# Optimization experiments

Hardware: AMD Instinct MI355X
Metric: run time of the kernel (lower is better)

## Reference

```python
import jax, jax.numpy as jnp
import numpy as np

B, T, D, K = 64, 4096, 90, 32
LOG2PI = 1.8378770664093453


def setup_inputs() -> dict:
    key = jax.random.key(0)
    k1, k2, k3, k4, k5 = jax.random.split(key, 5)
    X = jax.random.normal(k1, (B, T, D), dtype=jnp.float32)
    state_priors = jax.random.uniform(k2, (K,), dtype=jnp.float32)
    transition_matrix = jax.random.uniform(k3, (K, K), dtype=jnp.float32)
    mu = jax.random.normal(k4, (K, D), dtype=jnp.float32) * 0.5
    log_var = jax.random.normal(k5, (K, D), dtype=jnp.float32) * 0.1
    return {"X": X, "state_priors": state_priors,
            "transition_matrix": transition_matrix, "mu": mu, "log_var": log_var}


def _emission_logprobs(X, mu, log_var):
    # Diagonal-Gaussian log density per state: (B,T,K)
    # expand (x-mu)^2*inv_var to avoid materializing a (B,T,K,D) tensor
    inv_var = jnp.exp(-log_var)                                   # (K,D)
    quad = (jnp.einsum('btd,kd->btk', X * X, inv_var)
            - 2.0 * jnp.einsum('btd,kd->btk', X, mu * inv_var)
            + jnp.sum(mu * mu * inv_var, axis=-1))                # (B,T,K)
    return -0.5 * (quad + jnp.sum(log_var, axis=-1) + D * LOG2PI)


def reference(X, state_priors, transition_matrix, mu, log_var):
    log_A = jax.nn.log_softmax(transition_matrix, axis=1)   # (K,K)
    log_pi = jax.nn.log_softmax(state_priors, axis=0)       # (K,)
    em = _emission_logprobs(X, mu, log_var)                 # (B,T,K)

    log_alpha0 = log_pi + em[:, 0, :]                       # (B,K)

    def step(log_alpha, e_t):
        # log_alpha: (B,K), e_t: (B,K)
        la = e_t + jax.nn.logsumexp(log_alpha[:, :, None] + log_A[None], axis=1)
        return la, None

    em_rest = jnp.swapaxes(em[:, 1:, :], 0, 1)              # (T-1,B,K)
    log_alpha_T, _ = jax.lax.scan(step, log_alpha0, em_rest)
    # sum over subjects of logsumexp over states at final timestep
    return jnp.sum(jax.nn.logsumexp(log_alpha_T, axis=-1))
```

## Files before the change

kernel.cpp:

```cpp
#include <hip/hip_runtime.h>
#include <stdint.h>

#define B_ 64
#define T_ 4096
#define D_ 90
#define K_ 32
#define CH_ 32
#define F_  128

typedef float f32x16 __attribute__((ext_vector_type(16)));
typedef __bf16 bf16x8 __attribute__((ext_vector_type(8)));

#define WS_A     0
#define WS_PI    1024
#define WS_C0    1056
#define WS_WF    1088
#define WS_EACC  4160
#define WS_MS    12352
#define WS_E0    20544
#define WS_PE    21568
#define WS_PM    22080
#define WS_Q     284224

__device__ __forceinline__ int perm_r(int r) {
  int t2 = (r >> 2) & 3;
  return r + ((t2 == 1) ? 4 : (t2 == 2) ? -4 : 0);
}
__device__ __forceinline__ uint32_t pk2(float hi, float lo) {
  return __builtin_amdgcn_perm(__float_as_uint(hi), __float_as_uint(lo), 0x07060302u);
}
__device__ __forceinline__ uint32_t rnd_pk(float hi, float lo) {
  uint32_t uh = __float_as_uint(hi) + 0x8000u;
  uint32_t ul = __float_as_uint(lo) + 0x8000u;
  return __builtin_amdgcn_perm(uh, ul, 0x07060302u);
}
__device__ __forceinline__ float bf2f(ushort u) {
  return __uint_as_float(((uint32_t)u) << 16);
}
__device__ __forceinline__ bf16x8 mkbf(uint32_t a, uint32_t b, uint32_t c, uint32_t d) {
  union { uint32_t u[4]; bf16x8 v; } x;
  x.u[0] = a; x.u[1] = b; x.u[2] = c; x.u[3] = d;
  return x.v;
}

__global__ __launch_bounds__(1024) void prep_kernel(
    const float* __restrict__ priors, const float* __restrict__ trans,
    const float* __restrict__ mu, const float* __restrict__ lv,
    float* __restrict__ ws) {
  int tid = threadIdx.x;
  {
    float v = trans[tid];
    float m = v;
    #pragma unroll
    for (int mk = 16; mk; mk >>= 1) m = fmaxf(m, __shfl_xor(m, mk));
    float e = expf(v - m);
    float s = e;
    #pragma unroll
    for (int mk = 16; mk; mk >>= 1) s += __shfl_xor(s, mk);
    ws[WS_A + tid] = e / s;
  }
  if (tid < 32) {
    float v = priors[tid];
    float m = v;
    #pragma unroll
    for (int mk = 16; mk; mk >>= 1) m = fmaxf(m, __shfl_xor(m, mk));
    float e = expf(v - m);
    float s = e;
    #pragma unroll
    for (int mk = 16; mk; mk >>= 1) s += __shfl_xor(s, mk);
    ws[WS_PI + tid] = e / s;
  }
  for (int i = tid; i < 6144; i += 1024) {
    int j = i & 7, l = (i >> 3) & 63, cm = i >> 9;
    int c = cm >> 1, mat = cm & 1;
    int h = l >> 5, nn = l & 31;
    int d = 16 * c + 8 * h + j;
    float v = 0.0f;
    if (d < D_) {
      float ivd = expf(-lv[nn * D_ + d]);
      v = (mat == 0) ? -0.5f * ivd : mu[nn * D_ + d] * ivd;
    }
    ((ushort*)(ws + WS_WF))[i] = (ushort)((__float_as_uint(v) + 0x8000u) >> 16);
  }
  if (tid < 32) {
    float s = 0.0f;
    for (int d = 0; d < D_; ++d) {
      float l  = lv[tid * D_ + d];
      float iv = expf(-l);
      float m_ = mu[tid * D_ + d];
      s += m_ * m_ * iv + l;
    }
    ws[WS_C0 + tid] = -0.5f * (s + (float)D_ * 1.8378770664093453f);
  }
}

__global__ __launch_bounds__(256, 6) void fused_kernel(const float* __restrict__ X,
                                                       float* __restrict__ ws) {
  __shared__ ushort sh[4][32 * 104];
  int tid = threadIdx.x;
  int l = tid & 63, w = tid >> 6;
  int n = l & 31, h = l >> 5;
  int tB = blockIdx.x << 7;
  const float4* Xg = (const float4*)(X + (size_t)tB * D_);
  #pragma unroll
  for (int it = 0; it < 12; ++it) {
    int i = tid + (it << 8);
    if (i < 2880) {
      float4 v = Xg[i];
      int g = i / 720;
      int f = (i - g * 720) * 4;
      uint32_t d0 = rnd_pk(v.y, v.x);
      uint32_t d1 = rnd_pk(v.w, v.z);
      int r0 = f / 90;        int c0_ = f - r0 * 90;
      int r1 = (f + 2) / 90;  int c1_ = (f + 2) - r1 * 90;
      *(uint32_t*)&sh[g][r0 * 104 + c0_] = d0;
      *(uint32_t*)&sh[g][r1 * 104 + c1_] = d1;
    }
  }
  for (int i = tid; i < 896; i += 256) {
    int r = i / 7;
    int d = 90 + 2 * (i - r * 7);
    *(uint32_t*)&sh[r >> 5][(r & 31) * 104 + d] = 0u;
  }
  const uint4* wfp = (const uint4*)((const ushort*)(ws + WS_WF));
  uint4 wf[12];
  #pragma unroll
  for (int cm = 0; cm < 12; ++cm) wf[cm] = wfp[cm * 64 + l];
  float c0 = ws[WS_C0 + n];
  __syncthreads();

  int t0 = tB + (w << 5);
  int b  = t0 >> 12;
  int bc = t0 >> 5;
  const ushort* xrow = &sh[w][n * 104];
  f32x16 acc1, acc2;
  #pragma unroll
  for (int r = 0; r < 16; ++r) { acc1[r] = 0.0f; acc2[r] = 0.0f; }
  #pragma unroll
  for (int c = 0; c < 6; ++c) {
    union { uint4 u; bf16x8 v; } xb;
    xb.u = *(const uint4*)(xrow + 16 * c + 8 * h);
    float x[8];
    #pragma unroll
    for (int j = 0; j < 8; ++j) {
      uint32_t uu = ((const uint32_t*)&xb.u)[j >> 1];
      x[j] = bf2f((j & 1) ? (ushort)(uu >> 16) : (ushort)(uu & 0xFFFF));
    }
    union { uint32_t u[4]; bf16x8 v; } x2b;
    #pragma unroll
    for (int r = 0; r < 4; ++r)
      x2b.u[r] = rnd_pk(x[2*r+1] * x[2*r+1], x[2*r] * x[2*r]);
    union { uint4 u; bf16x8 v; } w2, w1;
    w2.u = wf[c * 2]; w1.u = wf[c * 2 + 1];
    acc1 = __builtin_amdgcn_mfma_f32_32x32x16_bf16(xb.v,  w1.v, acc1, 0, 0, 0);
    acc2 = __builtin_amdgcn_mfma_f32_32x32x16_bf16(x2b.v, w2.v, acc2, 0, 0, 0);
  }
  float em[16], mrow[16];
  #pragma unroll
  for (int r = 0; r < 16; ++r) {
    float v = acc1[r] + acc2[r] + c0;
    em[r] = v;
    float m = v;
    #pragma unroll
    for (int mk = 1; mk <= 16; mk <<= 1) m = fmaxf(m, __shfl_xor(m, mk));
    mrow[r] = m;
  }
  ushort* Ew = sh[w];
  #pragma unroll
  for (int q = 0; q < 4; ++q) {
    float e0 = exp2f((em[4*q]   - mrow[4*q])   * 1.44269504088896f);
    float e1 = exp2f((em[4*q+1] - mrow[4*q+1]) * 1.44269504088896f);
    float e2 = exp2f((em[4*q+2] - mrow[4*q+2]) * 1.44269504088896f);
    float e3 = exp2f((em[4*q+3] - mrow[4*q+3]) * 1.44269504088896f);
    uint2 d;
    d.x = rnd_pk(e1, e0);
    d.y = rnd_pk(e3, e2);
    *(uint2*)(Ew + n * 40 + 8 * q + 4 * h) = d;
    if (q == 0 && h == 0 && (t0 & (T_ - 1)) == 0)
      ((ushort*)(ws + WS_E0))[b * K_ + n] = (ushort)(d.x & 0xFFFF);
  }
  float msum = 0.0f;
  #pragma unroll
  for (int r = 0; r < 16; ++r) msum += mrow[r];
  msum += __shfl_xor(msum, 32);
  if (l == 0) ws[WS_MS + bc] = msum;

  int col = perm_r(n);
  const float* A = ws + WS_A;
  float astat[16];
  #pragma unroll
  for (int j = 0; j < 8; ++j) {
    astat[j]     = A[(8 * h + j) * K_ + col];
    astat[8 + j] = A[(16 + 8 * h + j) * K_ + col];
  }
  uint32_t q[8];
  #pragma unroll
  for (int r = 0; r < 4; ++r) {
    int s0 = 8 * h + 2 * r;
    uint32_t lo = (s0 == n)     ? 0x3F80u : 0u;
    uint32_t hi = (s0 + 1 == n) ? 0x3F80u : 0u;
    q[r] = lo | (hi << 16);
    int s2 = s0 + 16;
    lo = (s2 == n)     ? 0x3F80u : 0u;
    hi = (s2 + 1 == n) ? 0x3F80u : 0u;
    q[4 + r] = lo | (hi << 16);
  }
  int eacc = 0;
  const f32x16 z = {0.f,0.f,0.f,0.f,0.f,0.f,0.f,0.f,0.f,0.f,0.f,0.f,0.f,0.f,0.f,0.f};
  f32x16 acc;
  #pragma unroll
  for (int r = 0; r < 16; ++r) acc[r] = 0.0f;

  auto step = [&](float e0) {
    uint32_t au[8];
    #pragma unroll
    for (int r = 0; r < 4; ++r) {
      au[r]     = pk2(astat[2 * r + 1] * e0, astat[2 * r] * e0);
      au[4 + r] = pk2(astat[8 + 2 * r + 1] * e0, astat[8 + 2 * r] * e0);
    }
    bf16x8 alo = mkbf(au[0], au[1], au[2], au[3]);
    bf16x8 ahi = mkbf(au[4], au[5], au[6], au[7]);
    bf16x8 qlo = mkbf(q[0], q[1], q[2], q[3]);
    bf16x8 qhi = mkbf(q[4], q[5], q[6], q[7]);
    acc = __builtin_amdgcn_mfma_f32_32x32x16_bf16(alo, qlo, z, 0, 0, 0);
    acc = __builtin_amdgcn_mfma_f32_32x32x16_bf16(ahi, qhi, acc, 0, 0, 0);
    #pragma unroll
    for (int r = 0; r < 4; ++r) {
      q[r]     = pk2(acc[2 * r + 1], acc[2 * r]);
      q[4 + r] = pk2(acc[8 + 2 * r + 1], acc[8 + 2 * r]);
    }
  };
  auto renorm = [&]() {
    float m = acc[0];
    #pragma unroll
    for (int r = 1; r < 16; ++r) m = fmaxf(m, acc[r]);
    #pragma unroll
    for (int mk = 1; mk <= 32; mk <<= 1) m = fmaxf(m, __shfl_xor(m, mk));
    int ex;
    frexpf(m, &ex);
    float sc = ldexpf(1.0f, -ex);
    eacc += ex;
    #pragma unroll
    for (int r = 0; r < 16; ++r) acc[r] *= sc;
    #pragma unroll
    for (int r = 0; r < 4; ++r) {
      q[r]     = pk2(acc[2 * r + 1], acc[2 * r]);
      q[4 + r] = pk2(acc[8 + 2 * r + 1], acc[8 + 2 * r]);
    }
  };

  const ushort* Eb = sh[w] + col * 40;
  int g0 = 0;
  if ((t0 & (T_ - 1)) == 0) {
    uint4 ev = *(const uint4*)(Eb);
    #pragma unroll
    for (int j = 1; j < 8; ++j) {
      uint32_t u = ((const uint32_t*)&ev)[j >> 1];
      step(bf2f((j & 1) ? (ushort)(u >> 16) : (ushort)(u & 0xFFFF)));
    }
    renorm();
    g0 = 1;
  }
  for (int g = g0; g < CH_ / 8; ++g) {
    uint4 ev = *(const uint4*)(Eb + 8 * g);
    #pragma unroll
    for (int j = 0; j < 8; ++j) {
      uint32_t u = ((const uint32_t*)&ev)[j >> 1];
      step(bf2f((j & 1) ? (ushort)(u >> 16) : (ushort)(u & 0xFFFF)));
    }
    renorm();
  }
  ushort* Qo = (ushort*)(ws + WS_Q) + (size_t)bc * (K_ * K_);
  #pragma unroll
  for (int r = 0; r < 16; ++r) {
    int m_ = (r & 3) + 8 * (r >> 2) + 4 * h;
    Qo[perm_r(m_) * K_ + n] = (ushort)(__float_as_uint(acc[r]) >> 16);
  }
  if (l == 0) ((int*)ws)[WS_EACC + bc] = eacc;
}

__global__ __launch_bounds__(64) void combine1_kernel(float* __restrict__ ws) {
  int l = threadIdx.x;
  int h = l >> 5, n = l & 31;
  int bw = blockIdx.x;
  int b = bw >> 3, w = bw & 7;
  int row = perm_r(n);
  const ushort* Qb = (const ushort*)(ws + WS_Q) + (size_t)(b * F_ + w * 16) * (K_ * K_);
  int eacc;
  {
    const int* ea = ((const int*)ws) + WS_EACC + b * F_ + w * 16;
    int v = (l < 16) ? ea[l] : 0;
    #pragma unroll
    for (int mk = 1; mk <= 8; mk <<= 1) v += __shfl_xor(v, mk);
    eacc = __shfl(v, 0);
  }
  uint32_t q[8];
  #pragma unroll
  for (int r = 0; r < 4; ++r) {
    int s0 = 8 * h + 2 * r;
    uint32_t lo = (s0 == n)     ? 0x3F80u : 0u;
    uint32_t hi = (s0 + 1 == n) ? 0x3F80u : 0u;
    q[r] = lo | (hi << 16);
    int s2 = s0 + 16;
    lo = (s2 == n)     ? 0x3F80u : 0u;
    hi = (s2 + 1 == n) ? 0x3F80u : 0u;
    q[4 + r] = lo | (hi << 16);
  }
  f32x16 acc;
  #pragma unroll
  for (int r = 0; r < 16; ++r) acc[r] = 0.0f;
  const f32x16 z = {0.f,0.f,0.f,0.f,0.f,0.f,0.f,0.f,0.f,0.f,0.f,0.f,0.f,0.f,0.f,0.f};

  auto lmul = [&](uint4 lo, uint4 hi) {
    bf16x8 alo = mkbf(lo.x, lo.y, lo.z, lo.w);
    bf16x8 ahi = mkbf(hi.x, hi.y, hi.z, hi.w);
    bf16x8 qlo = mkbf(q[0], q[1], q[2], q[3]);
    bf16x8 qhi = mkbf(q[4], q[5], q[6], q[7]);
    acc = __builtin_amdgcn_mfma_f32_32x32x16_bf16(alo, qlo, z, 0, 0, 0);
    acc = __builtin_amdgcn_mfma_f32_32x32x16_bf16(ahi, qhi, acc, 0, 0, 0);
    #pragma unroll
    for (int r = 0; r < 4; ++r) {
      q[r]     = pk2(acc[2 * r + 1], acc[2 * r]);
      q[4 + r] = pk2(acc[8 + 2 * r + 1], acc[8 + 2 * r]);
    }
  };
  auto renorm = [&]() {
    float m = acc[0];
    #pragma unroll
    for (int r = 1; r < 16; ++r) m = fmaxf(m, acc[r]);
    #pragma unroll
    for (int mk = 1; mk <= 32; mk <<= 1) m = fmaxf(m, __shfl_xor(m, mk));
    int ex;
    frexpf(m, &ex);
    float sc = ldexpf(1.0f, -ex);
    eacc += ex;
    #pragma unroll
    for (int r = 0; r < 16; ++r) acc[r] *= sc;
    #pragma unroll
    for (int r = 0; r < 4; ++r) {
      q[r]     = pk2(acc[2 * r + 1], acc[2 * r]);
      q[4 + r] = pk2(acc[8 + 2 * r + 1], acc[8 + 2 * r]);
    }
  };

  uint4 rlo[4], rhi[4];
  #pragma unroll
  for (int p = 0; p < 4; ++p) {
    const ushort* Mc = Qb + (size_t)p * (K_ * K_) + row * K_;
    rlo[p] = *(const uint4*)(Mc + 8 * h);
    rhi[p] = *(const uint4*)(Mc + 16 + 8 * h);
  }
  #pragma unroll
  for (int c = 0; c < 16; ++c) {
    lmul(rlo[c & 3], rhi[c & 3]);
    if (c + 4 < 16) {
      const ushort* Mc = Qb + (size_t)(c + 4) * (K_ * K_) + row * K_;
      rlo[c & 3] = *(const uint4*)(Mc + 8 * h);
      rhi[c & 3] = *(const uint4*)(Mc + 16 + 8 * h);
    }
    if ((c & 3) == 3) renorm();
  }
  ushort* pmq = (ushort*)(ws + WS_PM) + (size_t)bw * (K_ * K_);
  #pragma unroll
  for (int r = 0; r < 16; ++r) {
    int m_ = (r & 3) + 8 * (r >> 2) + 4 * h;
    pmq[perm_r(m_) * K_ + n] = (ushort)(__float_as_uint(acc[r]) >> 16);
  }
  if (l == 0) ((int*)ws)[WS_PE + bw] = eacc;
}

__global__ __launch_bounds__(64) void combine2_kernel(float* __restrict__ ws,
                                                      float* __restrict__ out) {
  int l = threadIdx.x;
  int h = l >> 5, n = l & 31;
  int b = blockIdx.x;
  int row = perm_r(n);
  float alpha0 = ws[WS_PI + n] * bf2f(((const ushort*)(ws + WS_E0))[b * K_ + n]);
  float msm = ws[WS_MS + b * 128 + l] + ws[WS_MS + b * 128 + 64 + l];
  uint32_t q[8];
  #pragma unroll
  for (int r = 0; r < 4; ++r) {
    int s0 = 8 * h + 2 * r;
    uint32_t lo = (s0 == n)     ? 0x3F80u : 0u;
    uint32_t hi = (s0 + 1 == n) ? 0x3F80u : 0u;
    q[r] = lo | (hi << 16);
    int s2 = s0 + 16;
    lo = (s2 == n)     ? 0x3F80u : 0u;
    hi = (s2 + 1 == n) ? 0x3F80u : 0u;
    q[4 + r] = lo | (hi << 16);
  }
  f32x16 acc;
  #pragma unroll
  for (int r = 0; r < 16; ++r) acc[r] = 0.0f;
  const f32x16 z = {0.f,0.f,0.f,0.f,0.f,0.f,0.f,0.f,0.f,0.f,0.f,0.f,0.f,0.f,0.f,0.f};
  const ushort* pmq = (const ushort*)(ws + WS_PM) + (size_t)b * 8 * (K_ * K_);
  #pragma unroll
  for (int p = 0; p < 8; ++p) {
    const ushort* base = pmq + p * (K_ * K_) + row * K_;
    uint4 lo = *(const uint4*)(base + 8 * h);
    uint4 hi = *(const uint4*)(base + 16 + 8 * h);
    bf16x8 alo = mkbf(lo.x, lo.y, lo.z, lo.w);
    bf16x8 ahi = mkbf(hi.x, hi.y, hi.z, hi.w);
    bf16x8 qlo = mkbf(q[0], q[1], q[2], q[3]);
    bf16x8 qhi = mkbf(q[4], q[5], q[6], q[7]);
    acc = __builtin_amdgcn_mfma_f32_32x32x16_bf16(alo, qlo, z, 0, 0, 0);
    acc = __builtin_amdgcn_mfma_f32_32x32x16_bf16(ahi, qhi, acc, 0, 0, 0);
    #pragma unroll
    for (int r = 0; r < 4; ++r) {
      q[r]     = pk2(acc[2 * r + 1], acc[2 * r]);
      q[4 + r] = pk2(acc[8 + 2 * r + 1], acc[8 + 2 * r]);
    }
  }
  int et = (l < 8) ? ((const int*)ws)[WS_PE + b * 8 + l] : 0;
  #pragma unroll
  for (int mk = 1; mk <= 4; mk <<= 1) et += __shfl_xor(et, mk);
  et = __shfl(et, 0);
  float part = 0.0f;
  #pragma unroll
  for (int r = 0; r < 16; ++r) part += acc[r];
  part *= alpha0;
  #pragma unroll
  for (int mk = 1; mk <= 32; mk <<= 1) part += __shfl_xor(part, mk);
  #pragma unroll
  for (int mk = 32; mk; mk >>= 1) msm += __shfl_xor(msm, mk);
  if (l == 0) {
    float res = logf(part) + (float)et * 0.69314718055994531f + msm;
    atomicAdd(out, res);
  }
}

extern "C" void kernel_launch(void* const* d_in, const int* in_sizes, int n_in,
                              void* d_out, int out_size, void* d_ws, size_t ws_size,
                              hipStream_t stream) {
  (void)in_sizes; (void)n_in; (void)out_size; (void)ws_size;
  const float* X      = (const float*)d_in[0];
  const float* priors = (const float*)d_in[1];
  const float* trans  = (const float*)d_in[2];
  const float* mu     = (const float*)d_in[3];
  const float* lv     = (const float*)d_in[4];
  float* ws  = (float*)d_ws;
  float* out = (float*)d_out;
  hipMemsetAsync(out, 0, sizeof(float), stream);
  prep_kernel<<<1, 1024, 0, stream>>>(priors, trans, mu, lv, ws);
  fused_kernel<<<B_ * T_ / 128, 256, 0, stream>>>(X, ws);
  combine1_kernel<<<B_ * 8, 64, 0, stream>>>(ws);
  combine2_kernel<<<B_, 64, 0, stream>>>(ws, out);
}
```

Before: 185.7 us.

## Fold first combine level into fused kernel and merge combine stages

The fused kernel now multiplies the four per-warp 32x32 chunk transfer matrices inside each block through shared memory. It writes one matrix per block, cutting global workspace traffic and removing the combine1 launch. A single 256-thread combine kernel per batch reduces 32 block matrices in two levels. X is loaded directly from global memory into MFMA operands instead of staging through shared memory, the memset is folded into the kernel, and occupancy is raised to 8 blocks per SIMD. The changes add a block-wide sync plus serial tail work on warp 0, and bring uncoalesced strided X loads.

```diff
diff --git a/kernel.cpp b/kernel.cpp
--- a/kernel.cpp
+++ b/kernel.cpp
@@ -7,6 +7,7 @@
 #define K_ 32
 #define CH_ 32
 #define F_  128
+#define NB_ 2048
 
 typedef float f32x16 __attribute__((ext_vector_type(16)));
 typedef __bf16 bf16x8 __attribute__((ext_vector_type(8)));
@@ -18,9 +19,7 @@
 #define WS_EACC  4160
 #define WS_MS    12352
 #define WS_E0    20544
-#define WS_PE    21568
-#define WS_PM    22080
-#define WS_Q     284224
+#define WS_Q2    22080
 
 __device__ __forceinline__ int perm_r(int r) {
   int t2 = (r >> 2) & 3;
@@ -94,64 +93,41 @@
   }
 }
 
-__global__ __launch_bounds__(256, 6) void fused_kernel(const float* __restrict__ X,
-                                                       float* __restrict__ ws) {
-  __shared__ ushort sh[4][32 * 104];
+__global__ __launch_bounds__(256, 8) void fused_kernel(const float* __restrict__ X,
+                                                       float* __restrict__ ws,
+                                                       float* __restrict__ out) {
+  __shared__ __align__(16) ushort sh[4][1280];
+  __shared__ float msb[4];
+  __shared__ int   peb[4];
   int tid = threadIdx.x;
   int l = tid & 63, w = tid >> 6;
   int n = l & 31, h = l >> 5;
   int tB = blockIdx.x << 7;
-  const float4* Xg = (const float4*)(X + (size_t)tB * D_);
-  #pragma unroll
-  for (int it = 0; it < 12; ++it) {
-    int i = tid + (it << 8);
-    if (i < 2880) {
-      float4 v = Xg[i];
-      int g = i / 720;
-      int f = (i - g * 720) * 4;
-      uint32_t d0 = rnd_pk(v.y, v.x);
-      uint32_t d1 = rnd_pk(v.w, v.z);
-      int r0 = f / 90;        int c0_ = f - r0 * 90;
-      int r1 = (f + 2) / 90;  int c1_ = (f + 2) - r1 * 90;
-      *(uint32_t*)&sh[g][r0 * 104 + c0_] = d0;
-      *(uint32_t*)&sh[g][r1 * 104 + c1_] = d1;
-    }
-  }
-  for (int i = tid; i < 896; i += 256) {
-    int r = i / 7;
-    int d = 90 + 2 * (i - r * 7);
-    *(uint32_t*)&sh[r >> 5][(r & 31) * 104 + d] = 0u;
-  }
-  const uint4* wfp = (const uint4*)((const ushort*)(ws + WS_WF));
-  uint4 wf[12];
-  #pragma unroll
-  for (int cm = 0; cm < 12; ++cm) wf[cm] = wfp[cm * 64 + l];
-  float c0 = ws[WS_C0 + n];
-  __syncthreads();
-
   int t0 = tB + (w << 5);
   int b  = t0 >> 12;
-  int bc = t0 >> 5;
-  const ushort* xrow = &sh[w][n * 104];
+  if (blockIdx.x == 0 && tid == 0) *out = 0.0f;
+
+  const float* xr = X + (size_t)(t0 + n) * D_;
+  const uint4* wfp = (const uint4*)((const ushort*)(ws + WS_WF));
+  float c0 = ws[WS_C0 + n];
   f32x16 acc1, acc2;
   #pragma unroll
   for (int r = 0; r < 16; ++r) { acc1[r] = 0.0f; acc2[r] = 0.0f; }
   #pragma unroll
   for (int c = 0; c < 6; ++c) {
-    union { uint4 u; bf16x8 v; } xb;
-    xb.u = *(const uint4*)(xrow + 16 * c + 8 * h);
-    float x[8];
-    #pragma unroll
-    for (int j = 0; j < 8; ++j) {
-      uint32_t uu = ((const uint32_t*)&xb.u)[j >> 1];
-      x[j] = bf2f((j & 1) ? (ushort)(uu >> 16) : (ushort)(uu & 0xFFFF));
-    }
-    union { uint32_t u[4]; bf16x8 v; } x2b;
-    #pragma unroll
-    for (int r = 0; r < 4; ++r)
-      x2b.u[r] = rnd_pk(x[2*r+1] * x[2*r+1], x[2*r] * x[2*r]);
-    union { uint4 u; bf16x8 v; } w2, w1;
-    w2.u = wf[c * 2]; w1.u = wf[c * 2 + 1];
+    int s = 16 * c + 8 * h;
+    union { uint32_t u[4]; bf16x8 v; } xb, x2b;
+    #pragma unroll
+    for (int p = 0; p < 4; ++p) {
+      float2 v2;
+      if (s + 2 * p < D_) v2 = *(const float2*)(xr + s + 2 * p);
+      else { v2.x = 0.0f; v2.y = 0.0f; }
+      xb.u[p]  = rnd_pk(v2.y, v2.x);
+      x2b.u[p] = rnd_pk(v2.y * v2.y, v2.x * v2.x);
+    }
+    union { uint4 u; bf16x8 v; } w1, w2;
+    w2.u = wfp[(2 * c) * 64 + l];
+    w1.u = wfp[(2 * c + 1) * 64 + l];
     acc1 = __builtin_amdgcn_mfma_f32_32x32x16_bf16(xb.v,  w1.v, acc1, 0, 0, 0);
     acc2 = __builtin_amdgcn_mfma_f32_32x32x16_bf16(x2b.v, w2.v, acc2, 0, 0, 0);
   }
@@ -183,7 +159,7 @@
   #pragma unroll
   for (int r = 0; r < 16; ++r) msum += mrow[r];
   msum += __shfl_xor(msum, 32);
-  if (l == 0) ws[WS_MS + bc] = msum;
+  if (l == 0) msb[w] = msum;
 
   int col = perm_r(n);
   const float* A = ws + WS_A;
@@ -230,6 +206,19 @@
       q[4 + r] = pk2(acc[8 + 2 * r + 1], acc[8 + 2 * r]);
     }
   };
+  auto lmul = [&](uint4 lo, uint4 hi) {
+    bf16x8 alo = mkbf(lo.x, lo.y, lo.z, lo.w);
+    bf16x8 ahi = mkbf(hi.x, hi.y, hi.z, hi.w);
+    bf16x8 qlo = mkbf(q[0], q[1], q[2], q[3]);
+    bf16x8 qhi = mkbf(q[4], q[5], q[6], q[7]);
+    acc = __builtin_amdgcn_mfma_f32_32x32x16_bf16(alo, qlo, z, 0, 0, 0);
+    acc = __builtin_amdgcn_mfma_f32_32x32x16_bf16(ahi, qhi, acc, 0, 0, 0);
+    #pragma unroll
+    for (int r = 0; r < 4; ++r) {
+      q[r]     = pk2(acc[2 * r + 1], acc[2 * r]);
+      q[4 + r] = pk2(acc[8 + 2 * r + 1], acc[8 + 2 * r]);
+    }
+  };
   auto renorm = [&]() {
     float m = acc[0];
     #pragma unroll
@@ -270,31 +259,16 @@
     }
     renorm();
   }
-  ushort* Qo = (ushort*)(ws + WS_Q) + (size_t)bc * (K_ * K_);
+  ushort* Qw = sh[w];
   #pragma unroll
   for (int r = 0; r < 16; ++r) {
     int m_ = (r & 3) + 8 * (r >> 2) + 4 * h;
-    Qo[perm_r(m_) * K_ + n] = (ushort)(__float_as_uint(acc[r]) >> 16);
-  }
-  if (l == 0) ((int*)ws)[WS_EACC + bc] = eacc;
-}
-
-__global__ __launch_bounds__(64) void combine1_kernel(float* __restrict__ ws) {
-  int l = threadIdx.x;
-  int h = l >> 5, n = l & 31;
-  int bw = blockIdx.x;
-  int b = bw >> 3, w = bw & 7;
-  int row = perm_r(n);
-  const ushort* Qb = (const ushort*)(ws + WS_Q) + (size_t)(b * F_ + w * 16) * (K_ * K_);
-  int eacc;
-  {
-    const int* ea = ((const int*)ws) + WS_EACC + b * F_ + w * 16;
-    int v = (l < 16) ? ea[l] : 0;
-    #pragma unroll
-    for (int mk = 1; mk <= 8; mk <<= 1) v += __shfl_xor(v, mk);
-    eacc = __shfl(v, 0);
-  }
-  uint32_t q[8];
+    Qw[perm_r(m_) * 40 + n] = (ushort)(__float_as_uint(acc[r]) >> 16);
+  }
+  if (l == 0) peb[w] = eacc;
+  __syncthreads();
+  if (w != 0) return;
+
   #pragma unroll
   for (int r = 0; r < 4; ++r) {
     int s0 = 8 * h + 2 * r;
@@ -306,77 +280,45 @@
     hi = (s2 + 1 == n) ? 0x3F80u : 0u;
     q[4 + r] = lo | (hi << 16);
   }
-  f32x16 acc;
-  #pragma unroll
-  for (int r = 0; r < 16; ++r) acc[r] = 0.0f;
-  const f32x16 z = {0.f,0.f,0.f,0.f,0.f,0.f,0.f,0.f,0.f,0.f,0.f,0.f,0.f,0.f,0.f,0.f};
-
-  auto lmul = [&](uint4 lo, uint4 hi) {
-    bf16x8 alo = mkbf(lo.x, lo.y, lo.z, lo.w);
-    bf16x8 ahi = mkbf(hi.x, hi.y, hi.z, hi.w);
-    bf16x8 qlo = mkbf(q[0], q[1], q[2], q[3]);
-    bf16x8 qhi = mkbf(q[4], q[5], q[6], q[7]);
-    acc = __builtin_amdgcn_mfma_f32_32x32x16_bf16(alo, qlo, z, 0, 0, 0);
-    acc = __builtin_amdgcn_mfma_f32_32x32x16_bf16(ahi, qhi, acc, 0, 0, 0);
-    #pragma unroll
-    for (int r = 0; r < 4; ++r) {
-      q[r]     = pk2(acc[2 * r + 1], acc[2 * r]);
-      q[4 + r] = pk2(acc[8 + 2 * r + 1], acc[8 + 2 * r]);
-    }
-  };
-  auto renorm = [&]() {
-    float m = acc[0];
-    #pragma unroll
-    for (int r = 1; r < 16; ++r) m = fmaxf(m, acc[r]);
-    #pragma unroll
-    for (int mk = 1; mk <= 32; mk <<= 1) m = fmaxf(m, __shfl_xor(m, mk));
-    int ex;
-    frexpf(m, &ex);
-    float sc = ldexpf(1.0f, -ex);
-    eacc += ex;
-    #pragma unroll
-    for (int r = 0; r < 16; ++r) acc[r] *= sc;
-    #pragma unroll
-    for (int r = 0; r < 4; ++r) {
-      q[r]     = pk2(acc[2 * r + 1], acc[2 * r]);
-      q[4 + r] = pk2(acc[8 + 2 * r + 1], acc[8 + 2 * r]);
-    }
-  };
-
-  uint4 rlo[4], rhi[4];
+  eacc = peb[0] + peb[1] + peb[2] + peb[3];
+  float msm = msb[0] + msb[1] + msb[2] + msb[3];
   #pragma unroll
   for (int p = 0; p < 4; ++p) {
-    const ushort* Mc = Qb + (size_t)p * (K_ * K_) + row * K_;
-    rlo[p] = *(const uint4*)(Mc + 8 * h);
-    rhi[p] = *(const uint4*)(Mc + 16 + 8 * h);
-  }
-  #pragma unroll
-  for (int c = 0; c < 16; ++c) {
-    lmul(rlo[c & 3], rhi[c & 3]);
-    if (c + 4 < 16) {
-      const ushort* Mc = Qb + (size_t)(c + 4) * (K_ * K_) + row * K_;
-      rlo[c & 3] = *(const uint4*)(Mc + 8 * h);
-      rhi[c & 3] = *(const uint4*)(Mc + 16 + 8 * h);
-    }
-    if ((c & 3) == 3) renorm();
-  }
-  ushort* pmq = (ushort*)(ws + WS_PM) + (size_t)bw * (K_ * K_);
+    const ushort* base = sh[p] + col * 40;
+    uint4 lo = *(const uint4*)(base + 8 * h);
+    uint4 hi = *(const uint4*)(base + 16 + 8 * h);
+    lmul(lo, hi);
+  }
+  renorm();
+  ushort* Qo = (ushort*)(ws + WS_Q2) + (size_t)blockIdx.x * (K_ * K_);
   #pragma unroll
   for (int r = 0; r < 16; ++r) {
     int m_ = (r & 3) + 8 * (r >> 2) + 4 * h;
-    pmq[perm_r(m_) * K_ + n] = (ushort)(__float_as_uint(acc[r]) >> 16);
-  }
-  if (l == 0) ((int*)ws)[WS_PE + bw] = eacc;
-}
-
-__global__ __launch_bounds__(64) void combine2_kernel(float* __restrict__ ws,
+    Qo[perm_r(m_) * K_ + n] = (ushort)(__float_as_uint(acc[r]) >> 16);
+  }
+  if (l == 0) {
+    ((int*)ws)[WS_EACC + blockIdx.x] = eacc;
+    ws[WS_MS + blockIdx.x] = msm;
+  }
+}
+
+__global__ __launch_bounds__(256) void combine_kernel(float* __restrict__ ws,
                                                       float* __restrict__ out) {
-  int l = threadIdx.x;
+  __shared__ __align__(16) ushort pm[4][1280];
+  __shared__ int pe[4];
+  int tid = threadIdx.x;
+  int l = tid & 63, w = tid >> 6;
   int h = l >> 5, n = l & 31;
   int b = blockIdx.x;
   int row = perm_r(n);
-  float alpha0 = ws[WS_PI + n] * bf2f(((const ushort*)(ws + WS_E0))[b * K_ + n]);
-  float msm = ws[WS_MS + b * 128 + l] + ws[WS_MS + b * 128 + 64 + l];
+  int eacc;
+  {
+    const int* ea = ((const int*)ws) + WS_EACC + b * 32 + w * 8;
+    int v = (l < 8) ? ea[l] : 0;
+    #pragma unroll
+    for (int mk = 1; mk <= 4; mk <<= 1) v += __shfl_xor(v, mk);
+    eacc = __shfl(v, 0);
+  }
   uint32_t q[8];
   #pragma unroll
   for (int r = 0; r < 4; ++r) {
@@ -393,12 +335,8 @@
   #pragma unroll
   for (int r = 0; r < 16; ++r) acc[r] = 0.0f;
   const f32x16 z = {0.f,0.f,0.f,0.f,0.f,0.f,0.f,0.f,0.f,0.f,0.f,0.f,0.f,0.f,0.f,0.f};
-  const ushort* pmq = (const ushort*)(ws + WS_PM) + (size_t)b * 8 * (K_ * K_);
-  #pragma unroll
-  for (int p = 0; p < 8; ++p) {
-    const ushort* base = pmq + p * (K_ * K_) + row * K_;
-    uint4 lo = *(const uint4*)(base + 8 * h);
-    uint4 hi = *(const uint4*)(base + 16 + 8 * h);
+
+  auto lmul = [&](uint4 lo, uint4 hi) {
     bf16x8 alo = mkbf(lo.x, lo.y, lo.z, lo.w);
     bf16x8 ahi = mkbf(hi.x, hi.y, hi.z, hi.w);
     bf16x8 qlo = mkbf(q[0], q[1], q[2], q[3]);
@@ -410,19 +348,79 @@
       q[r]     = pk2(acc[2 * r + 1], acc[2 * r]);
       q[4 + r] = pk2(acc[8 + 2 * r + 1], acc[8 + 2 * r]);
     }
-  }
-  int et = (l < 8) ? ((const int*)ws)[WS_PE + b * 8 + l] : 0;
-  #pragma unroll
-  for (int mk = 1; mk <= 4; mk <<= 1) et += __shfl_xor(et, mk);
-  et = __shfl(et, 0);
+  };
+  auto renorm = [&]() {
+    float m = acc[0];
+    #pragma unroll
+    for (int r = 1; r < 16; ++r) m = fmaxf(m, acc[r]);
+    #pragma unroll
+    for (int mk = 1; mk <= 32; mk <<= 1) m = fmaxf(m, __shfl_xor(m, mk));
+    int ex;
+    frexpf(m, &ex);
+    float sc = ldexpf(1.0f, -ex);
+    eacc += ex;
+    #pragma unroll
+    for (int r = 0; r < 16; ++r) acc[r] *= sc;
+    #pragma unroll
+    for (int r = 0; r < 4; ++r) {
+      q[r]     = pk2(acc[2 * r + 1], acc[2 * r]);
+      q[4 + r] = pk2(acc[8 + 2 * r + 1], acc[8 + 2 * r]);
+    }
+  };
+
+  const ushort* Qb = (const ushort*)(ws + WS_Q2) + (size_t)(b * 32 + w * 8) * (K_ * K_);
+  #pragma unroll
+  for (int p = 0; p < 8; ++p) {
+    const ushort* Mc = Qb + (size_t)p * (K_ * K_) + row * K_;
+    uint4 lo = *(const uint4*)(Mc + 8 * h);
+    uint4 hi = *(const uint4*)(Mc + 16 + 8 * h);
+    lmul(lo, hi);
+    if ((p & 3) == 3) renorm();
+  }
+  #pragma unroll
+  for (int r = 0; r < 16; ++r) {
+    int m_ = (r & 3) + 8 * (r >> 2) + 4 * h;
+    pm[w][perm_r(m_) * 40 + n] = (ushort)(__float_as_uint(acc[r]) >> 16);
+  }
+  if (l == 0) pe[w] = eacc;
+  __syncthreads();
+  if (w != 0) return;
+
+  float alpha0 = ws[WS_PI + n] * bf2f(((const ushort*)(ws + WS_E0))[b * K_ + n]);
+  float msm;
+  {
+    float v = (l < 32) ? ws[WS_MS + b * 32 + l] : 0.0f;
+    #pragma unroll
+    for (int mk = 1; mk <= 32; mk <<= 1) v += __shfl_xor(v, mk);
+    msm = v;
+  }
+  #pragma unroll
+  for (int r = 0; r < 4; ++r) {
+    int s0 = 8 * h + 2 * r;
+    uint32_t lo = (s0 == n)     ? 0x3F80u : 0u;
+    uint32_t hi = (s0 + 1 == n) ? 0x3F80u : 0u;
+    q[r] = lo | (hi << 16);
+    int s2 = s0 + 16;
+    lo = (s2 == n)     ? 0x3F80u : 0u;
+    hi = (s2 + 1 == n) ? 0x3F80u : 0u;
+    q[4 + r] = lo | (hi << 16);
+  }
+  #pragma unroll
+  for (int r = 0; r < 16; ++r) acc[r] = 0.0f;
+  int et = pe[0] + pe[1] + pe[2] + pe[3];
+  #pragma unroll
+  for (int p = 0; p < 4; ++p) {
+    const ushort* base = pm[p] + row * 40;
+    uint4 lo = *(const uint4*)(base + 8 * h);
+    uint4 hi = *(const uint4*)(base + 16 + 8 * h);
+    lmul(lo, hi);
+  }
   float part = 0.0f;
   #pragma unroll
   for (int r = 0; r < 16; ++r) part += acc[r];
   part *= alpha0;
   #pragma unroll
   for (int mk = 1; mk <= 32; mk <<= 1) part += __shfl_xor(part, mk);
-  #pragma unroll
-  for (int mk = 32; mk; mk >>= 1) msm += __shfl_xor(msm, mk);
   if (l == 0) {
     float res = logf(part) + (float)et * 0.69314718055994531f + msm;
     atomicAdd(out, res);
@@ -440,9 +438,7 @@
   const float* lv     = (const float*)d_in[4];
   float* ws  = (float*)d_ws;
   float* out = (float*)d_out;
-  hipMemsetAsync(out, 0, sizeof(float), stream);
   prep_kernel<<<1, 1024, 0, stream>>>(priors, trans, mu, lv, ws);
-  fused_kernel<<<B_ * T_ / 128, 256, 0, stream>>>(X, ws);
-  combine1_kernel<<<B_ * 8, 64, 0, stream>>>(ws);
-  combine2_kernel<<<B_, 64, 0, stream>>>(ws, out);
-}
+  fused_kernel<<<NB_, 256, 0, stream>>>(X, ws, out);
+  combine_kernel<<<B_, 256, 0, stream>>>(ws, out);
+}
```

Result: slower. 192.6 us (+3.7%).
